# Kernel optimization log

Hardware: AMD Instinct MI355X
Metric: run time of the kernel (lower is better)

The kernel has to match this reference:

```python
import math
import jax, jax.numpy as jnp
import numpy as np

KS, UP, DOWN = 4, 2, 1
P1 = (KS - 1) // 2          # 1
P2 = KS - 1 - P1            # 2


def make_kernel(ks: int) -> jnp.ndarray:
    k = np.array([math.comb(ks - 1, i) for i in range(ks)], dtype=np.float32)
    k = k / k.sum()
    return jnp.asarray(np.outer(k, k))  # [ky, kx], separable binomial


def setup_inputs() -> dict:
    key = jax.random.key(0)
    imgs = jax.random.normal(key, (16, 128, 128, 128), dtype=jnp.float32)
    return {"imgs": imgs, "kernel": make_kernel(KS)}


def reference(imgs, kernel):
    # upfirdn2d: zero-insert upsample by UP, pad (P1,P2) each spatial side,
    # depthwise cross-correlate with `kernel`, downsample by DOWN.
    # lhs_dilation implements the zero-insert upsample without materializing it;
    # XLA applies padding after lhs dilation, matching pad-after-upsample.
    n, c, h, w = imgs.shape
    rhs = jnp.broadcast_to(kernel[None, None], (c, 1, kernel.shape[0], kernel.shape[1]))
    out = jax.lax.conv_general_dilated(
        imgs, rhs,
        window_strides=(DOWN, DOWN),
        padding=[(P1, P2), (P1, P2)],
        lhs_dilation=(UP, UP),
        dimension_numbers=("NCHW", "OIHW", "NCHW"),
        feature_group_count=c,
    )
    return out  # [N, C, H*UP, W*UP]
```

## Files before the change

kernel.cpp:

```cpp
#include <hip/hip_runtime.h>


#define IH 128
#define IW 128

typedef float f2 __attribute__((ext_vector_type(2)));
typedef float f4 __attribute__((ext_vector_type(4)));
typedef f4 uf4 __attribute__((aligned(4)));

__global__ __launch_bounds__(256) void blur_up2_vec(
    const float* __restrict__ in, const float* __restrict__ ker,
    float* __restrict__ out, int oh, int ow) {
    int bid = blockIdx.x;
    int lb  = (bid & 7) * (int)(gridDim.x >> 3) + (bid >> 3);
    int id  = lb * 256 + (int)threadIdx.x;

    int j  = id & 63;
    int iy = (id >> 6) & 127;
    int nc = id >> 13;

    const float* ib = in + ((size_t)nc << 14) + ((size_t)iy << 7) + (j << 1);

    f2 r0 = *reinterpret_cast<const f2*>(ib);
    float a = r0.x, b = r0.y;
    float e = (j < 63) ? ib[2] : 0.f;

    float c = 0.f, d = 0.f, f = 0.f;
    if (iy < IH - 1) {
        f2 r1 = *reinterpret_cast<const f2*>(ib + IW);
        c = r1.x; d = r1.y;
        f = (j < 63) ? ib[IW + 2] : 0.f;
    }

    float K00 = ker[0],  K01 = ker[1],  K02 = ker[2],  K03 = ker[3];
    float K10 = ker[4],  K11 = ker[5],  K12 = ker[6],  K13 = ker[7];
    float K20 = ker[8],  K21 = ker[9],  K22 = ker[10], K23 = ker[11];
    float K30 = ker[12], K31 = ker[13], K32 = ker[14], K33 = ker[15];

    f4 o0, o1;
    o0.x = K11 * a + K13 * b + K31 * c + K33 * d;
    o0.y = K10 * a + K12 * b + K30 * c + K32 * d;
    o0.z = K11 * b + K13 * e + K31 * d + K33 * f;
    o0.w = K10 * b + K12 * e + K30 * d + K32 * f;
    o1.x = K01 * a + K03 * b + K21 * c + K23 * d;
    o1.y = K00 * a + K02 * b + K20 * c + K22 * d;
    o1.z = K01 * b + K03 * e + K21 * d + K23 * f;
    o1.w = K00 * b + K02 * e + K20 * d + K22 * f;

    int oy = iy << 1, ox = j << 2;
    size_t ob = (size_t)nc * ((size_t)oh * ow) + (size_t)oy * ow + ox;
    bool odd = (oy + 1 < oh);

    if (ox + 3 < ow) {
        *reinterpret_cast<uf4*>(out + ob) = o0;
        if (odd) *reinterpret_cast<uf4*>(out + ob + ow) = o1;
    } else {
        int rem = ow - ox;
        if (rem > 0) out[ob] = o0.x;
        if (rem > 1) out[ob + 1] = o0.y;
        if (rem > 2) out[ob + 2] = o0.z;
        if (odd) {
            if (rem > 0) out[ob + ow] = o1.x;
            if (rem > 1) out[ob + ow + 1] = o1.y;
            if (rem > 2) out[ob + ow + 2] = o1.z;
        }
    }
}

extern "C" void kernel_launch(void* const* d_in, const int* in_sizes, int n_in,
                              void* d_out, int out_size, void* d_ws, size_t ws_size,
                              hipStream_t stream) {
    const float* imgs = (const float*)d_in[0];
    const float* ker  = (const float*)d_in[1];
    float* out        = (float*)d_out;

    const int NC = 16 * 128;
    int ohw = out_size / NC;
    int ow = (ohw == 256 * 256) ? 256 : 255;
    int oh = ow;

    int total  = NC * IH * (IW / 2);
    int blocks = total / 256;
    blur_up2_vec<<<blocks, 256, 0, stream>>>(imgs, ker, out, oh, ow);
}
```

Before: 640.4 us.

## Process four input rows per thread to reuse halo rows, use nontemporal stores

```diff
diff --git a/kernel.cpp b/kernel.cpp
--- a/kernel.cpp
+++ b/kernel.cpp
@@ -8,28 +8,32 @@
 typedef float f4 __attribute__((ext_vector_type(4)));
 typedef f4 uf4 __attribute__((aligned(4)));
 
-__global__ __launch_bounds__(256) void blur_up2_vec(
+__global__ __launch_bounds__(256) void blur_up2_band(
     const float* __restrict__ in, const float* __restrict__ ker,
     float* __restrict__ out, int oh, int ow) {
     int bid = blockIdx.x;
     int lb  = (bid & 7) * (int)(gridDim.x >> 3) + (bid >> 3);
     int id  = lb * 256 + (int)threadIdx.x;
 
-    int j  = id & 63;
-    int iy = (id >> 6) & 127;
-    int nc = id >> 13;
+    int j    = id & 63;
+    int band = (id >> 6) & 31;
+    int nc   = id >> 11;
 
-    const float* ib = in + ((size_t)nc << 14) + ((size_t)iy << 7) + (j << 1);
+    const float* ib = in + ((size_t)nc << 14) + (j << 1);
+    int y0 = band << 2;
+    bool jin = (j < 63);
 
-    f2 r0 = *reinterpret_cast<const f2*>(ib);
-    float a = r0.x, b = r0.y;
-    float e = (j < 63) ? ib[2] : 0.f;
-
-    float c = 0.f, d = 0.f, f = 0.f;
-    if (iy < IH - 1) {
-        f2 r1 = *reinterpret_cast<const f2*>(ib + IW);
-        c = r1.x; d = r1.y;
-        f = (j < 63) ? ib[IW + 2] : 0.f;
+    float A[5], B[5], E[5];
+#pragma unroll
+    for (int r = 0; r < 5; ++r) {
+        int y = y0 + r;
+        if (y < IH) {
+            f2 v = *reinterpret_cast<const f2*>(ib + ((size_t)y << 7));
+            A[r] = v.x; B[r] = v.y;
+            E[r] = jin ? ib[((size_t)y << 7) + 2] : 0.f;
+        } else {
+            A[r] = 0.f; B[r] = 0.f; E[r] = 0.f;
+        }
     }
 
     float K00 = ker[0],  K01 = ker[1],  K02 = ker[2],  K03 = ker[3];
@@ -37,32 +41,38 @@
     float K20 = ker[8],  K21 = ker[9],  K22 = ker[10], K23 = ker[11];
     float K30 = ker[12], K31 = ker[13], K32 = ker[14], K33 = ker[15];
 
-    f4 o0, o1;
-    o0.x = K11 * a + K13 * b + K31 * c + K33 * d;
-    o0.y = K10 * a + K12 * b + K30 * c + K32 * d;
-    o0.z = K11 * b + K13 * e + K31 * d + K33 * f;
-    o0.w = K10 * b + K12 * e + K30 * d + K32 * f;
-    o1.x = K01 * a + K03 * b + K21 * c + K23 * d;
-    o1.y = K00 * a + K02 * b + K20 * c + K22 * d;
-    o1.z = K01 * b + K03 * e + K21 * d + K23 * f;
-    o1.w = K00 * b + K02 * e + K20 * d + K22 * f;
+    size_t obase = (size_t)nc * ((size_t)oh * ow);
+    int ox  = j << 2;
+    int rem = ow - ox;
 
-    int oy = iy << 1, ox = j << 2;
-    size_t ob = (size_t)nc * ((size_t)oh * ow) + (size_t)oy * ow + ox;
-    bool odd = (oy + 1 < oh);
+#pragma unroll
+    for (int k = 0; k < 4; ++k) {
+        float a = A[k],     b = B[k],     e = E[k];
+        float c = A[k + 1], d = B[k + 1], f = E[k + 1];
 
-    if (ox + 3 < ow) {
-        *reinterpret_cast<uf4*>(out + ob) = o0;
-        if (odd) *reinterpret_cast<uf4*>(out + ob + ow) = o1;
-    } else {
-        int rem = ow - ox;
-        if (rem > 0) out[ob] = o0.x;
-        if (rem > 1) out[ob + 1] = o0.y;
-        if (rem > 2) out[ob + 2] = o0.z;
-        if (odd) {
-            if (rem > 0) out[ob + ow] = o1.x;
-            if (rem > 1) out[ob + ow + 1] = o1.y;
-            if (rem > 2) out[ob + ow + 2] = o1.z;
+        f4 o0, o1;
+        o0.x = K11 * a + K13 * b + K31 * c + K33 * d;
+        o0.y = K10 * a + K12 * b + K30 * c + K32 * d;
+        o0.z = K11 * b + K13 * e + K31 * d + K33 * f;
+        o0.w = K10 * b + K12 * e + K30 * d + K32 * f;
+        o1.x = K01 * a + K03 * b + K21 * c + K23 * d;
+        o1.y = K00 * a + K02 * b + K20 * c + K22 * d;
+        o1.z = K01 * b + K03 * e + K21 * d + K23 * f;
+        o1.w = K00 * b + K02 * e + K20 * d + K22 * f;
+
+        int oy = (y0 + k) << 1;
+        size_t ob = obase + (size_t)oy * ow + ox;
+        bool odd = (oy + 1 < oh);
+
+        if (rem >= 4) {
+            __builtin_nontemporal_store(o0, reinterpret_cast<uf4*>(out + ob));
+            if (odd)
+                __builtin_nontemporal_store(o1, reinterpret_cast<uf4*>(out + ob + ow));
+        } else {
+            out[ob] = o0.x; out[ob + 1] = o0.y; out[ob + 2] = o0.z;
+            if (odd) {
+                out[ob + ow] = o1.x; out[ob + ow + 1] = o1.y; out[ob + ow + 2] = o1.z;
+            }
         }
     }
 }
@@ -79,7 +89,7 @@
     int ow = (ohw == 256 * 256) ? 256 : 255;
     int oh = ow;
 
-    int total  = NC * IH * (IW / 2);
+    int total  = NC * 32 * 64;
     int blocks = total / 256;
-    blur_up2_vec<<<blocks, 256, 0, stream>>>(imgs, ker, out, oh, ow);
+    blur_up2_band<<<blocks, 256, 0, stream>>>(imgs, ker, out, oh, ow);
 }
```

New measurement: 632.7 us. No clear change (-1.2%).
